# Performance work log

Hardware: AMD Instinct MI355X
Metric: run time of the kernel (lower is better)

The kernel has to match this reference:

```python
import jax, jax.numpy as jnp
import numpy as np

# dims (match init_kwargs)
B, S, HID = 2, 2048, 2048
NH = 16
DN = 128   # qk_nope_head_dim
DR = 64    # qk_rope_head_dim
DV = 128   # v_head_dim
QLR = 1536 # q_lora_rank
KVLR = 512 # kv_lora_rank
QHD = DN + DR  # 192
ROPE_BASE = 10000.0
EPS = 1e-6


def rms_norm(x, w):
    # ZeroCenteredRMSNorm: weight is zero-centered, scale = (1 + w)
    var = jnp.mean(x * x, axis=-1, keepdims=True)
    return x * jax.lax.rsqrt(var + EPS) * (1.0 + w)


def rotate_half(x):
    d = x.shape[-1] // 2
    return jnp.concatenate([-x[..., d:], x[..., :d]], axis=-1)


def deinterleave(x):
    # rearrange '(d_pairs two) -> (two d_pairs)'
    return jnp.concatenate([x[..., 0::2], x[..., 1::2]], axis=-1)


def setup_inputs() -> dict:
    key = jax.random.key(0)
    ks = jax.random.split(key, 8)
    s = 0.02
    return {
        "hidden_states": jax.random.normal(ks[0], (B, S, HID), jnp.float32),
        "position_ids": jnp.arange(S, dtype=jnp.int32),
        "Wq_down": jax.random.normal(ks[1], (HID, QLR), jnp.float32) * s,
        "q_norm_w": jnp.zeros((QLR,), jnp.float32),
        "Wq_up": jax.random.normal(ks[2], (QLR, NH * QHD), jnp.float32) * s,
        "Wkv_down": jax.random.normal(ks[3], (HID, KVLR + DR), jnp.float32) * s,
        "kv_norm_w": jnp.zeros((KVLR,), jnp.float32),
        "Wkv_up": jax.random.normal(ks[4], (KVLR, NH * (DN + DV)), jnp.float32) * s,
        "W_gate": jax.random.normal(ks[5], (HID, NH * DV), jnp.float32) * s,
        "W_out": jax.random.normal(ks[6], (NH * DV, HID), jnp.float32) * s,
    }


def reference(hidden_states, position_ids, Wq_down, q_norm_w, Wq_up,
              Wkv_down, kv_norm_w, Wkv_up, W_gate, W_out):
    bsz, q_len, _ = hidden_states.shape
    pos = jnp.broadcast_to(position_ids[None, :], (bsz, q_len))  # [b,s]

    # Q path: down-proj -> RMSNorm -> up-proj -> [b,h,s,QHD]
    q = rms_norm(hidden_states @ Wq_down, q_norm_w) @ Wq_up
    q = q.reshape(bsz, q_len, NH, QHD).transpose(0, 2, 1, 3)
    q_nope, q_rope = q[..., :DN], q[..., DN:]

    # KV path: joint down-proj -> split latent / rope key
    ckv = hidden_states @ Wkv_down                     # [b,s,KVLR+DR]
    c_kv, k_rope = ckv[..., :KVLR], ckv[..., KVLR:]
    k_rope = k_rope[:, None, :, :]                     # [b,1,s,DR]
    kv = rms_norm(c_kv, kv_norm_w) @ Wkv_up            # [b,s,NH*(DN+DV)]
    kv = kv.reshape(bsz, q_len, NH, DN + DV).transpose(0, 2, 1, 3)
    k_nope, v = kv[..., :DN], kv[..., DN:]

    # partial RoPE on rope dims (with the '(pairs two)->(two pairs)' permute)
    inv_freq = 1.0 / (ROPE_BASE ** (jnp.arange(0, DR, 2, dtype=jnp.float32) / DR))
    freqs = pos[..., None].astype(jnp.float32) * inv_freq  # [b,s,DR/2]
    emb = jnp.concatenate([freqs, freqs], axis=-1)          # [b,s,DR]
    cos = jnp.cos(emb)[:, None, :, :]                       # [b,1,s,DR]
    sin = jnp.sin(emb)[:, None, :, :]
    q_r = deinterleave(q_rope)
    k_r = deinterleave(k_rope)
    q_r = q_r * cos + rotate_half(q_r) * sin
    k_r = k_r * cos + rotate_half(k_r) * sin

    query = jnp.concatenate([q_nope, q_r], axis=-1)                       # [b,h,s,QHD]
    key = jnp.concatenate([k_nope, jnp.broadcast_to(k_r, k_nope.shape[:-1] + (DR,))], axis=-1)

    scores = jnp.einsum('bhqd,bhkd->bhqk', query, key) / np.sqrt(QHD)
    attn = jax.nn.softmax(scores, axis=-1)
    out = jnp.einsum('bhqk,bhkd->bhqd', attn, v)                          # [b,h,s,DV]
    out = out.transpose(0, 2, 1, 3)                                       # [b,s,h,DV]

    gate = jax.nn.sigmoid(hidden_states @ W_gate).reshape(bsz, q_len, NH, DV)
    out = (out * gate).reshape(bsz, q_len, NH * DV)
    return out @ W_out
```

## Files before the change

### kernel.cpp

```cpp
#include <hip/hip_runtime.h>
#include <math.h>

#define BT 2
#define SL 2048
#define HIDN 2048
#define NHEADS 16
#define DNOPE 128
#define DROPE 64
#define DVAL 128
#define QHEAD 192
#define QLRANK 1536
#define KVLRANK 512
#define TTOK (BT * SL)
#define FN 4224
#define FC_CKV 1536
#define FC_ROPE 2048
#define FC_GATE 2176

typedef unsigned short u16;
typedef u16 u16x4 __attribute__((ext_vector_type(4)));
typedef u16 u16x8 __attribute__((ext_vector_type(8)));
typedef short bf16x8 __attribute__((ext_vector_type(8)));
typedef float f32x4 __attribute__((ext_vector_type(4)));

__device__ __forceinline__ u16 f2b(float f) {
    union { float f; unsigned u; } v; v.f = f;
    unsigned r = v.u + 0x7FFFu + ((v.u >> 16) & 1u);
    return (u16)(r >> 16);
}
__device__ __forceinline__ float b2f(u16 h) {
    union { unsigned u; float f; } v; v.u = ((unsigned)h) << 16;
    return v.f;
}
__device__ __forceinline__ float fexp2(float x) {
    float r;
    asm("v_exp_f32 %0, %1" : "=v"(r) : "v"(x));
    return r;
}

__device__ __forceinline__ void gl2lds16(const u16* g, u16* l) {
    __builtin_amdgcn_global_load_lds((const __attribute__((address_space(1))) unsigned int*)g,
                                     (__attribute__((address_space(3))) unsigned int*)l, 16, 0, 0);
}

__device__ __forceinline__ void tcast_tile(const float* __restrict__ in, u16* __restrict__ out,
                                           int R, int C, int tx, int ty, int t) {
    __shared__ u16 tile[64][72];
    const int c0 = tx * 64, r0 = ty * 64;
    const int tr = t >> 4, tc4 = (t & 15) * 4;
#pragma unroll
    for (int i = 0; i < 4; ++i) {
        const int r = tr + i * 16;
        const float4 v = *(const float4*)&in[(size_t)(r0 + r) * C + c0 + tc4];
        u16x4 u;
        u.x = f2b(v.x); u.y = f2b(v.y); u.z = f2b(v.z); u.w = f2b(v.w);
        *(u16x4*)&tile[r][tc4] = u;
    }
    __syncthreads();
#pragma unroll
    for (int i = 0; i < 4; ++i) {
        const int rr = tr + i * 16;
        u16x4 u;
        u.x = tile[tc4 + 0][rr];
        u.y = tile[tc4 + 1][rr];
        u.z = tile[tc4 + 2][rr];
        u.w = tile[tc4 + 3][rr];
        *(u16x4*)&out[(size_t)(c0 + rr) * R + r0 + tc4] = u;
    }
}

__global__ __launch_bounds__(256) void precast_k(
    const float* __restrict__ Wq_down, const float* __restrict__ Wq_up,
    const float* __restrict__ Wkv_down, const float* __restrict__ Wkv_up,
    const float* __restrict__ W_gate, const float* __restrict__ W_out,
    const float* __restrict__ hs, u16* __restrict__ wqd_t, u16* __restrict__ wqu_t,
    u16* __restrict__ wkvd_t, u16* __restrict__ wkvu_t, u16* __restrict__ wg_t,
    u16* __restrict__ wo_t, u16* __restrict__ hs16) {
    const int tid = blockIdx.x;
    const int t = threadIdx.x;
    if (tid >= 4768) {
        int i = (tid - 4768) * 256 + t;
        for (; i < TTOK * HIDN / 4; i += 2048 * 256) {
            const float4 v = ((const float4*)hs)[i];
            u16x4 u;
            u.x = f2b(v.x); u.y = f2b(v.y); u.z = f2b(v.z); u.w = f2b(v.w);
            ((u16x4*)hs16)[i] = u;
        }
        return;
    }
    if (tid < 768) {
        tcast_tile(Wq_down, wqd_t, 2048, 1536, tid % 24, tid / 24, t);
    } else if (tid < 1920) {
        const int i = tid - 768;
        tcast_tile(Wq_up, wqu_t, 1536, 3072, i % 48, i / 48, t);
    } else if (tid < 2208) {
        const int i = tid - 1920;
        tcast_tile(Wkv_down, wkvd_t, 2048, 576, i % 9, i / 9, t);
    } else if (tid < 2720) {
        const int i = tid - 2208;
        tcast_tile(Wkv_up, wkvu_t, 512, 4096, i % 64, i / 64, t);
    } else if (tid < 3744) {
        const int i = tid - 2720;
        tcast_tile(W_gate, wg_t, 2048, 2048, i % 32, i / 32, t);
    } else {
        const int i = tid - 3744;
        tcast_tile(W_out, wo_t, 2048, 2048, i % 32, i / 32, t);
    }
}

template <int MODE>
__global__ __launch_bounds__(256) void gemm_bf16_k(const u16* __restrict__ A,
                                                   const u16* __restrict__ Bt,
                                                   void* __restrict__ Cv, u16* __restrict__ C2,
                                                   int M, int N, int K) {
    __shared__ u16 As[128 * 64];
    __shared__ u16 Bs[128 * 64];
    const int t = threadIdx.x;
    const int nx = gridDim.x;
    const int bid = blockIdx.x + nx * blockIdx.y;
    const int cpx = (nx * gridDim.y) >> 3;
    const int swz = (bid & 7) * cpx + (bid >> 3);
    const int bn = (swz % nx) * 128, bm = (swz / nx) * 128;
    const int w = t >> 6, lane = t & 63;
    const int wr = (w >> 1) * 64, wc = (w & 1) * 64;
    const int lr = lane & 15, lg = lane >> 4;

    const int srow = w * 32 + (lane >> 3);
    const int scol = ((lane & 7) ^ ((lane >> 3) & 7)) * 8;
    const u16* Ag = A + (size_t)(bm + srow) * K + scol;
    const u16* Bg = Bt + (size_t)(bn + srow) * K + scol;
    u16* Asl = As + w * 2048;
    u16* Bsl = Bs + w * 2048;

    f32x4 acc[4][4];
#pragma unroll
    for (int i = 0; i < 4; ++i)
#pragma unroll
        for (int j = 0; j < 4; ++j) acc[i][j] = 0.f;

    for (int k0 = 0; k0 < K; k0 += 64) {
        __syncthreads();
#pragma unroll
        for (int j = 0; j < 4; ++j) gl2lds16(Ag + (size_t)(j * 8) * K + k0, Asl + j * 512);
#pragma unroll
        for (int j = 0; j < 4; ++j) gl2lds16(Bg + (size_t)(j * 8) * K + k0, Bsl + j * 512);
        __syncthreads();
#pragma unroll
        for (int kk = 0; kk < 2; ++kk) {
            bf16x8 af[4], bfr[4];
#pragma unroll
            for (int mi = 0; mi < 4; ++mi) {
                const int row = wr + mi * 16 + lr;
                const int idx = (row * 64 + kk * 32 + lg * 8) ^ ((row & 7) << 3);
                af[mi] = *(const bf16x8*)&As[idx];
            }
#pragma unroll
            for (int ni = 0; ni < 4; ++ni) {
                const int row = wc + ni * 16 + lr;
                const int idx = (row * 64 + kk * 32 + lg * 8) ^ ((row & 7) << 3);
                bfr[ni] = *(const bf16x8*)&Bs[idx];
            }
#pragma unroll
            for (int mi = 0; mi < 4; ++mi)
#pragma unroll
                for (int ni = 0; ni < 4; ++ni)
                    acc[mi][ni] = __builtin_amdgcn_mfma_f32_16x16x32_bf16(af[mi], bfr[ni],
                                                                          acc[mi][ni], 0, 0, 0);
        }
    }
#pragma unroll
    for (int mi = 0; mi < 4; ++mi)
#pragma unroll
        for (int ni = 0; ni < 4; ++ni) {
            const int row0 = bm + wr + mi * 16 + lg * 4;
            const int col = bn + wc + ni * 16 + lr;
            if (MODE == 3) {
                const int h = col >> 8, cd = col & 255;
                if (cd < 128) {
#pragma unroll
                    for (int r = 0; r < 4; ++r)
                        ((u16*)Cv)[(size_t)(row0 + r) * 2048 + h * 128 + cd] =
                            f2b(acc[mi][ni][r]);
                } else {
                    u16x4 pk;
                    pk.x = f2b(acc[mi][ni][0]);
                    pk.y = f2b(acc[mi][ni][1]);
                    pk.z = f2b(acc[mi][ni][2]);
                    pk.w = f2b(acc[mi][ni][3]);
                    const int bb = row0 >> 11;
                    *(u16x4*)&C2[((size_t)((bb * 16 + h) * 128 + (cd - 128))) * SL +
                                 (row0 & (SL - 1))] = pk;
                }
            } else {
#pragma unroll
                for (int r = 0; r < 4; ++r) {
                    float v = acc[mi][ni][r];
                    if (MODE == 2 && col >= FC_GATE) v = 1.f / (1.f + __expf(-v));
                    if (MODE == 1)
                        ((float*)Cv)[(size_t)(row0 + r) * N + col] = v;
                    else
                        ((u16*)Cv)[(size_t)(row0 + r) * N + col] = f2b(v);
                }
            }
        }
}

__global__ __launch_bounds__(256) void rms2_k(const u16* __restrict__ fout,
                                              const float* __restrict__ qw,
                                              const float* __restrict__ kw, u16* __restrict__ qn,
                                              u16* __restrict__ kvn) {
    const int rid = blockIdx.x;
    const bool isq = rid < TTOK;
    const int row = isq ? rid : rid - TTOK;
    const int n = isq ? QLRANK : KVLRANK;
    const u16* x = fout + (size_t)row * FN + (isq ? 0 : FC_CKV);
    const float* w = isq ? qw : kw;
    u16* y = isq ? (qn + (size_t)row * QLRANK) : (kvn + (size_t)row * KVLRANK);
    const int t = threadIdx.x;
    float ss = 0.f;
    for (int d = t * 4; d < n; d += 1024) {
        const u16x4 u = *(const u16x4*)&x[d];
        const float a = b2f(u.x), b = b2f(u.y), c = b2f(u.z), e = b2f(u.w);
        ss += a * a + b * b + c * c + e * e;
    }
    ss += __shfl_down(ss, 32);
    ss += __shfl_down(ss, 16);
    ss += __shfl_down(ss, 8);
    ss += __shfl_down(ss, 4);
    ss += __shfl_down(ss, 2);
    ss += __shfl_down(ss, 1);
    __shared__ float red[5];
    if ((t & 63) == 0) red[t >> 6] = ss;
    __syncthreads();
    if (t == 0) red[4] = rsqrtf((red[0] + red[1] + red[2] + red[3]) / (float)n + 1e-6f);
    __syncthreads();
    const float sc = red[4];
    for (int d = t * 4; d < n; d += 1024) {
        const u16x4 u = *(const u16x4*)&x[d];
        const float4 wv = *(const float4*)&w[d];
        u16x4 o;
        o.x = f2b(b2f(u.x) * sc * (1.f + wv.x));
        o.y = f2b(b2f(u.y) * sc * (1.f + wv.y));
        o.z = f2b(b2f(u.z) * sc * (1.f + wv.z));
        o.w = f2b(b2f(u.w) * sc * (1.f + wv.w));
        *(u16x4*)&y[d] = o;
    }
}

__global__ __launch_bounds__(64) void rope_k(u16* __restrict__ q, const u16* __restrict__ fout,
                                             u16* __restrict__ kr, const int* __restrict__ pos_ids) {
    const int tok = blockIdx.x * 2 + (threadIdx.x >> 5);
    const int j = threadIdx.x & 31;
    const int s = tok & (SL - 1);
    const float pos = (float)pos_ids[s];
    const float inv = 1.f / powf(10000.f, (float)(2 * j) / 64.f);
    const float f = pos * inv;
    const float c = cosf(f), sn = sinf(f);
    const u16* kc = fout + (size_t)tok * FN + FC_ROPE;
    const unsigned kp = *(const unsigned*)&kc[2 * j];
    const float ke = b2f((u16)(kp & 0xffff)), ko = b2f((u16)(kp >> 16));
    kr[tok * 64 + j] = f2b(ke * c - ko * sn);
    kr[tok * 64 + 32 + j] = f2b(ko * c + ke * sn);
#pragma unroll
    for (int h = 0; h < NHEADS; ++h) {
        u16* qb = q + (size_t)tok * (NHEADS * QHEAD) + h * QHEAD + DNOPE;
        const unsigned qp = *(const unsigned*)&qb[2 * j];
        const float qe = b2f((u16)(qp & 0xffff)), qo = b2f((u16)(qp >> 16));
        qb[j] = f2b(qe * c - qo * sn);
        qb[32 + j] = f2b(qo * c + qe * sn);
    }
}

#define PSTR 76
__global__ __launch_bounds__(256, 2) void mla_attn_k(const u16* __restrict__ qbuf,
                                                     const u16* __restrict__ knope,
                                                     const u16* __restrict__ kr,
                                                     const u16* __restrict__ vT,
                                                     const u16* __restrict__ gateb,
                                                     u16* __restrict__ outg) {
    __shared__ u16 Ks[64 * 200];
    __shared__ u16 Vt[128 * 72];
    __shared__ u16 Ps[4 * 32 * PSTR];
    const int bh = blockIdx.x;
    const int b = bh >> 4, h = bh & 15;
    const int q0 = blockIdx.y * 128;
    const int t = threadIdx.x, w = t >> 6, lane = t & 63;
    const int lr = lane & 15, lg = lane >> 4;
    const float qs = 0.07216878364870322f * 1.4426950408889634f;
    const float THR = 8.f * 1.4426950408889634f;

    int kRow[6], kC8[6];
#pragma unroll
    for (int c = 0; c < 6; ++c) {
        const int i = t + c * 256;
        kRow[c] = i / 24;
        kC8[c] = (i % 24) * 8;
    }
    int vRow[4], vC8[4];
#pragma unroll
    for (int c = 0; c < 4; ++c) {
        const int i = t + c * 256;
        vRow[c] = i >> 3;
        vC8[c] = (i & 7) * 8;
    }

    bf16x8 aq[2][6];
#pragma unroll
    for (int mi = 0; mi < 2; ++mi) {
        const int qrow = b * SL + q0 + w * 32 + mi * 16 + lr;
#pragma unroll
        for (int ks = 0; ks < 6; ++ks) {
            const u16x8 raw = *(const u16x8*)&qbuf[(size_t)qrow * (NHEADS * QHEAD) + h * QHEAD +
                                                   ks * 32 + lg * 8];
            bf16x8 o;
#pragma unroll
            for (int j = 0; j < 8; ++j) o[j] = (short)f2b(b2f(raw[j]) * qs);
            aq[mi][ks] = o;
        }
    }

    f32x4 O[2][8];
#pragma unroll
    for (int mi = 0; mi < 2; ++mi)
#pragma unroll
        for (int df = 0; df < 8; ++df) O[mi][df] = 0.f;
    float m[2][4], l[2][4];
#pragma unroll
    for (int mi = 0; mi < 2; ++mi)
#pragma unroll
        for (int r = 0; r < 4; ++r) {
            m[mi][r] = -INFINITY;
            l[mi][r] = 0.f;
        }

    u16x8 kreg[6], vreg[4];
#define ATTN_ISSUE_K(K0)                                                                     \
    {                                                                                        \
        _Pragma("unroll") for (int c = 0; c < 6; ++c) {                                      \
            const int tok = b * SL + (K0) + kRow[c];                                         \
            kreg[c] = (kC8[c] < 128)                                                         \
                          ? *(const u16x8*)&knope[(size_t)tok * 2048 + h * 128 + kC8[c]]     \
                          : *(const u16x8*)&kr[(size_t)tok * 64 + (kC8[c] - 128)];           \
        }                                                                                    \
    }
#define ATTN_ISSUE_V(K0)                                                                     \
    {                                                                                        \
        _Pragma("unroll") for (int c = 0; c < 4; ++c)                                        \
            vreg[c] = *(const u16x8*)&vT[(size_t)(bh * 128 + vRow[c]) * SL + (K0) + vC8[c]]; \
    }

    ATTN_ISSUE_K(0);
    ATTN_ISSUE_V(0);

    for (int it = 0; it < SL / 64; ++it) {
        __syncthreads();
#pragma unroll
        for (int c = 0; c < 6; ++c) *(u16x8*)&Ks[kRow[c] * 200 + kC8[c]] = kreg[c];
#pragma unroll
        for (int c = 0; c < 4; ++c) *(u16x8*)&Vt[vRow[c] * 72 + vC8[c]] = vreg[c];
        __syncthreads();
        const bool more = (it + 1) < SL / 64;
        const int kn = (it + 1) * 64;
        if (more) ATTN_ISSUE_K(kn);

        f32x4 s[2][4];
#pragma unroll
        for (int mi = 0; mi < 2; ++mi)
#pragma unroll
            for (int nf = 0; nf < 4; ++nf) s[mi][nf] = 0.f;
#pragma unroll
        for (int ks = 0; ks < 6; ++ks) {
#pragma unroll
            for (int nf = 0; nf < 4; ++nf) {
                const bf16x8 bk = *(const bf16x8*)&Ks[(nf * 16 + lr) * 200 + ks * 32 + lg * 8];
                s[0][nf] = __builtin_amdgcn_mfma_f32_16x16x32_bf16(aq[0][ks], bk, s[0][nf], 0, 0, 0);
                s[1][nf] = __builtin_amdgcn_mfma_f32_16x16x32_bf16(aq[1][ks], bk, s[1][nf], 0, 0, 0);
            }
        }

        float lmv[2][4];
        float growth = -INFINITY;
#pragma unroll
        for (int mi = 0; mi < 2; ++mi)
#pragma unroll
            for (int r = 0; r < 4; ++r) {
                float lm = fmaxf(fmaxf(s[mi][0][r], s[mi][1][r]), fmaxf(s[mi][2][r], s[mi][3][r]));
                lm = fmaxf(lm, __shfl_xor(lm, 1));
                lm = fmaxf(lm, __shfl_xor(lm, 2));
                lm = fmaxf(lm, __shfl_xor(lm, 4));
                lm = fmaxf(lm, __shfl_xor(lm, 8));
                lmv[mi][r] = lm;
                growth = fmaxf(growth, lm - m[mi][r]);
            }
        const bool skip = __all(growth <= THR);

#pragma unroll
        for (int mi = 0; mi < 2; ++mi) {
            const int pb = w * 32 * PSTR + mi * 16 * PSTR;
#pragma unroll
            for (int r = 0; r < 4; ++r) {
                const float mn = skip ? m[mi][r] : fmaxf(m[mi][r], lmv[mi][r]);
                float p0 = fexp2(s[mi][0][r] - mn);
                float p1 = fexp2(s[mi][1][r] - mn);
                float p2 = fexp2(s[mi][2][r] - mn);
                float p3 = fexp2(s[mi][3][r] - mn);
                float ps = (p0 + p1) + (p2 + p3);
                ps += __shfl_xor(ps, 1);
                ps += __shfl_xor(ps, 2);
                ps += __shfl_xor(ps, 4);
                ps += __shfl_xor(ps, 8);
                if (skip) {
                    l[mi][r] += ps;
                } else {
                    const float al = fexp2(m[mi][r] - mn);
                    l[mi][r] = l[mi][r] * al + ps;
                    m[mi][r] = mn;
#pragma unroll
                    for (int df = 0; df < 8; ++df) O[mi][df][r] *= al;
                }
                const int prow = pb + (lg * 4 + r) * PSTR + lr;
                Ps[prow] = f2b(p0);
                Ps[prow + 16] = f2b(p1);
                Ps[prow + 32] = f2b(p2);
                Ps[prow + 48] = f2b(p3);
            }
        }

        if (more) ATTN_ISSUE_V(kn);

        bf16x8 pa[2][2];
#pragma unroll
        for (int mi = 0; mi < 2; ++mi)
#pragma unroll
            for (int ks2 = 0; ks2 < 2; ++ks2)
                pa[mi][ks2] =
                    *(const bf16x8*)&Ps[w * 32 * PSTR + (mi * 16 + lr) * PSTR + ks2 * 32 + lg * 8];
#pragma unroll
        for (int df = 0; df < 8; ++df)
#pragma unroll
            for (int ks2 = 0; ks2 < 2; ++ks2) {
                const bf16x8 bv = *(const bf16x8*)&Vt[(df * 16 + lr) * 72 + ks2 * 32 + lg * 8];
                O[0][df] = __builtin_amdgcn_mfma_f32_16x16x32_bf16(pa[0][ks2], bv, O[0][df], 0, 0, 0);
                O[1][df] = __builtin_amdgcn_mfma_f32_16x16x32_bf16(pa[1][ks2], bv, O[1][df], 0, 0, 0);
            }
    }
#pragma unroll
    for (int mi = 0; mi < 2; ++mi) {
        float invl[4];
#pragma unroll
        for (int r = 0; r < 4; ++r) invl[r] = 1.f / l[mi][r];
#pragma unroll
        for (int df = 0; df < 8; ++df)
#pragma unroll
            for (int r = 0; r < 4; ++r) {
                const int qq = b * SL + q0 + w * 32 + mi * 16 + lg * 4 + r;
                const int col = h * DVAL + df * 16 + lr;
                const float o = O[mi][df][r] * invl[r];
                const float g = b2f(gateb[(size_t)qq * FN + col]);
                outg[(size_t)qq * (NHEADS * DVAL) + col] = f2b(o * g);
            }
    }
}

extern "C" void kernel_launch(void* const* d_in, const int* in_sizes, int n_in, void* d_out,
                              int out_size, void* d_ws, size_t ws_size, hipStream_t stream) {
    const float* hs = (const float*)d_in[0];
    const int* pos = (const int*)d_in[1];
    const float* Wq_down = (const float*)d_in[2];
    const float* q_norm_w = (const float*)d_in[3];
    const float* Wq_up = (const float*)d_in[4];
    const float* Wkv_down = (const float*)d_in[5];
    const float* kv_norm_w = (const float*)d_in[6];
    const float* Wkv_up = (const float*)d_in[7];
    const float* W_gate = (const float*)d_in[8];
    const float* W_out = (const float*)d_in[9];
    float* out = (float*)d_out;

    u16* p = (u16*)d_ws;
    u16* hs16 = p;      p += (size_t)TTOK * HIDN;
    u16* wdown_t = p;   p += (size_t)FN * HIDN;
    u16* wqd_t = wdown_t;
    u16* wkvd_t = wdown_t + (size_t)QLRANK * HIDN;
    u16* wg_t = wdown_t + (size_t)FC_GATE * HIDN;
    u16* wqu_t = p;     p += (size_t)(NHEADS * QHEAD) * QLRANK;
    u16* wkvu_t = p;    p += (size_t)(NHEADS * 256) * KVLRANK;
    u16* wo_t = p;      p += (size_t)HIDN * (NHEADS * DVAL);
    u16* fout = p;      p += (size_t)TTOK * FN;
    u16* qdownN = p;    p += (size_t)TTOK * QLRANK;
    u16* qbuf = p;      p += (size_t)TTOK * (NHEADS * QHEAD);
    u16* kvn = p;       p += (size_t)TTOK * KVLRANK;
    u16* knope = p;     p += (size_t)TTOK * (NHEADS * DNOPE);
    u16* krb = p;       p += (size_t)TTOK * DROPE;
    u16* vTg = p;       p += (size_t)32 * 128 * SL;
    u16* outg = p;      p += (size_t)TTOK * (NHEADS * DVAL);

    const dim3 blk(256);

    precast_k<<<dim3(6816), blk, 0, stream>>>(Wq_down, Wq_up, Wkv_down, Wkv_up, W_gate, W_out, hs,
                                              wqd_t, wqu_t, wkvd_t, wkvu_t, wg_t, wo_t, hs16);

    gemm_bf16_k<2><<<dim3(FN / 128, TTOK / 128), blk, 0, stream>>>(hs16, wdown_t, fout, nullptr,
                                                                   TTOK, FN, HIDN);
    rms2_k<<<dim3(2 * TTOK), blk, 0, stream>>>(fout, q_norm_w, kv_norm_w, qdownN, kvn);
    gemm_bf16_k<0><<<dim3((NHEADS * QHEAD) / 128, TTOK / 128), blk, 0, stream>>>(
        qdownN, wqu_t, qbuf, nullptr, TTOK, NHEADS * QHEAD, QLRANK);
    gemm_bf16_k<3><<<dim3((NHEADS * 256) / 128, TTOK / 128), blk, 0, stream>>>(
        kvn, wkvu_t, knope, vTg, TTOK, NHEADS * 256, KVLRANK);
    rope_k<<<dim3(TTOK / 2), dim3(64), 0, stream>>>(qbuf, fout, krb, pos);

    mla_attn_k<<<dim3(32, SL / 128), blk, 0, stream>>>(qbuf, knope, krb, vTg, fout + FC_GATE, outg);

    gemm_bf16_k<1><<<dim3(HIDN / 128, TTOK / 128), blk, 0, stream>>>(outg, wo_t, out, nullptr, TTOK,
                                                                     HIDN, NHEADS * DVAL);
}
```

Measured before the change: 466.0 us.

## Use 256x128 tiles with double-buffered LDS prefetch in bf16 GEMMs

Replaces the 128x128, 256-thread GEMM with a 256x128, 512-thread kernel. LDS is double-buffered so the next K tile's global-to-LDS loads are in flight while MFMAs run on the current tile, with explicit vmcnt waits and barriers. This targets exposed load latency and the two barriers per K step that the old single-buffer loop paid. In exchange, LDS use per block grows to 96KB and the grid gets fewer blocks (e.g. 16x16 for the output projection), which may hurt occupancy and wave balance across CUs.

```diff
diff --git a/kernel.cpp b/kernel.cpp
--- a/kernel.cpp
+++ b/kernel.cpp
@@ -109,71 +109,91 @@
 }
 
 template <int MODE>
-__global__ __launch_bounds__(256) void gemm_bf16_k(const u16* __restrict__ A,
-                                                   const u16* __restrict__ Bt,
-                                                   void* __restrict__ Cv, u16* __restrict__ C2,
-                                                   int M, int N, int K) {
-    __shared__ u16 As[128 * 64];
-    __shared__ u16 Bs[128 * 64];
+__global__ __launch_bounds__(512) void gemm256_k(const u16* __restrict__ A,
+                                                 const u16* __restrict__ Bt,
+                                                 void* __restrict__ Cv, u16* __restrict__ C2,
+                                                 int M, int N, int K) {
+    __shared__ u16 As[2][256 * 64];
+    __shared__ u16 Bs[2][128 * 64];
     const int t = threadIdx.x;
     const int nx = gridDim.x;
     const int bid = blockIdx.x + nx * blockIdx.y;
     const int cpx = (nx * gridDim.y) >> 3;
     const int swz = (bid & 7) * cpx + (bid >> 3);
-    const int bn = (swz % nx) * 128, bm = (swz / nx) * 128;
+    const int bn = (swz % nx) * 128, bm = (swz / nx) * 256;
     const int w = t >> 6, lane = t & 63;
-    const int wr = (w >> 1) * 64, wc = (w & 1) * 64;
+    const int wrow = (w >> 2) * 128, wcol = (w & 3) * 32;
     const int lr = lane & 15, lg = lane >> 4;
 
-    const int srow = w * 32 + (lane >> 3);
-    const int scol = ((lane & 7) ^ ((lane >> 3) & 7)) * 8;
-    const u16* Ag = A + (size_t)(bm + srow) * K + scol;
-    const u16* Bg = Bt + (size_t)(bn + srow) * K + scol;
-    u16* Asl = As + w * 2048;
-    u16* Bsl = Bs + w * 2048;
-
-    f32x4 acc[4][4];
-#pragma unroll
-    for (int i = 0; i < 4; ++i)
-#pragma unroll
-        for (int j = 0; j < 4; ++j) acc[i][j] = 0.f;
-
-    for (int k0 = 0; k0 < K; k0 += 64) {
-        __syncthreads();
-#pragma unroll
-        for (int j = 0; j < 4; ++j) gl2lds16(Ag + (size_t)(j * 8) * K + k0, Asl + j * 512);
-#pragma unroll
-        for (int j = 0; j < 4; ++j) gl2lds16(Bg + (size_t)(j * 8) * K + k0, Bsl + j * 512);
-        __syncthreads();
+    const int lrow = lane >> 3;
+    const int scol = ((lane & 7) ^ (lrow & 7)) * 8;
+    const u16* Ag = A + (size_t)(bm + w * 32 + lrow) * K + scol;
+    const u16* Bg = Bt + (size_t)(bn + w * 16 + lrow) * K + scol;
+
+#define STAGE256(kt, bsel)                                                           \
+    {                                                                                \
+        u16* ad = &As[bsel][w * 2048];                                               \
+        u16* bd = &Bs[bsel][w * 1024];                                               \
+        _Pragma("unroll") for (int j = 0; j < 4; ++j)                                \
+            gl2lds16(Ag + (size_t)(j * 8) * K + (size_t)(kt) * 64, ad + j * 512);    \
+        _Pragma("unroll") for (int j = 0; j < 2; ++j)                                \
+            gl2lds16(Bg + (size_t)(j * 8) * K + (size_t)(kt) * 64, bd + j * 512);    \
+    }
+
+    f32x4 acc[8][2];
+#pragma unroll
+    for (int i = 0; i < 8; ++i)
+#pragma unroll
+        for (int j = 0; j < 2; ++j) acc[i][j] = 0.f;
+
+    const int nt = K >> 6;
+    STAGE256(0, 0);
+    for (int kt = 0; kt < nt; ++kt) {
+        const int cur = kt & 1;
+        if (kt + 1 < nt) {
+            STAGE256(kt + 1, cur ^ 1);
+            asm volatile("s_waitcnt vmcnt(6)" ::: "memory");
+        } else {
+            asm volatile("s_waitcnt vmcnt(0)" ::: "memory");
+        }
+        __builtin_amdgcn_sched_barrier(0);
+        __builtin_amdgcn_s_barrier();
+        __builtin_amdgcn_sched_barrier(0);
 #pragma unroll
         for (int kk = 0; kk < 2; ++kk) {
-            bf16x8 af[4], bfr[4];
-#pragma unroll
-            for (int mi = 0; mi < 4; ++mi) {
-                const int row = wr + mi * 16 + lr;
+            bf16x8 af[8], bfr[2];
+#pragma unroll
+            for (int mi = 0; mi < 8; ++mi) {
+                const int row = wrow + mi * 16 + lr;
                 const int idx = (row * 64 + kk * 32 + lg * 8) ^ ((row & 7) << 3);
-                af[mi] = *(const bf16x8*)&As[idx];
-            }
-#pragma unroll
-            for (int ni = 0; ni < 4; ++ni) {
-                const int row = wc + ni * 16 + lr;
+                af[mi] = *(const bf16x8*)&As[cur][idx];
+            }
+#pragma unroll
+            for (int ni = 0; ni < 2; ++ni) {
+                const int row = wcol + ni * 16 + lr;
                 const int idx = (row * 64 + kk * 32 + lg * 8) ^ ((row & 7) << 3);
-                bfr[ni] = *(const bf16x8*)&Bs[idx];
-            }
-#pragma unroll
-            for (int mi = 0; mi < 4; ++mi)
-#pragma unroll
-                for (int ni = 0; ni < 4; ++ni)
+                bfr[ni] = *(const bf16x8*)&Bs[cur][idx];
+            }
+#pragma unroll
+            for (int mi = 0; mi < 8; ++mi)
+#pragma unroll
+                for (int ni = 0; ni < 2; ++ni)
                     acc[mi][ni] = __builtin_amdgcn_mfma_f32_16x16x32_bf16(af[mi], bfr[ni],
                                                                           acc[mi][ni], 0, 0, 0);
         }
-    }
-#pragma unroll
-    for (int mi = 0; mi < 4; ++mi)
-#pragma unroll
-        for (int ni = 0; ni < 4; ++ni) {
-            const int row0 = bm + wr + mi * 16 + lg * 4;
-            const int col = bn + wc + ni * 16 + lr;
+        asm volatile("s_waitcnt lgkmcnt(0)" ::: "memory");
+        __builtin_amdgcn_sched_barrier(0);
+        __builtin_amdgcn_s_barrier();
+        __builtin_amdgcn_sched_barrier(0);
+    }
+#undef STAGE256
+
+#pragma unroll
+    for (int mi = 0; mi < 8; ++mi)
+#pragma unroll
+        for (int ni = 0; ni < 2; ++ni) {
+            const int row0 = bm + wrow + mi * 16 + lg * 4;
+            const int col = bn + wcol + ni * 16 + lr;
             if (MODE == 3) {
                 const int h = col >> 8, cd = col & 255;
                 if (cd < 128) {
@@ -495,21 +515,22 @@
     u16* outg = p;      p += (size_t)TTOK * (NHEADS * DVAL);
 
     const dim3 blk(256);
+    const dim3 blk512(512);
 
     precast_k<<<dim3(6816), blk, 0, stream>>>(Wq_down, Wq_up, Wkv_down, Wkv_up, W_gate, W_out, hs,
                                               wqd_t, wqu_t, wkvd_t, wkvu_t, wg_t, wo_t, hs16);
 
-    gemm_bf16_k<2><<<dim3(FN / 128, TTOK / 128), blk, 0, stream>>>(hs16, wdown_t, fout, nullptr,
-                                                                   TTOK, FN, HIDN);
+    gemm256_k<2><<<dim3(FN / 128, TTOK / 256), blk512, 0, stream>>>(hs16, wdown_t, fout, nullptr,
+                                                                    TTOK, FN, HIDN);
     rms2_k<<<dim3(2 * TTOK), blk, 0, stream>>>(fout, q_norm_w, kv_norm_w, qdownN, kvn);
-    gemm_bf16_k<0><<<dim3((NHEADS * QHEAD) / 128, TTOK / 128), blk, 0, stream>>>(
+    gemm256_k<0><<<dim3((NHEADS * QHEAD) / 128, TTOK / 256), blk512, 0, stream>>>(
         qdownN, wqu_t, qbuf, nullptr, TTOK, NHEADS * QHEAD, QLRANK);
-    gemm_bf16_k<3><<<dim3((NHEADS * 256) / 128, TTOK / 128), blk, 0, stream>>>(
+    gemm256_k<3><<<dim3((NHEADS * 256) / 128, TTOK / 256), blk512, 0, stream>>>(
         kvn, wkvu_t, knope, vTg, TTOK, NHEADS * 256, KVLRANK);
     rope_k<<<dim3(TTOK / 2), dim3(64), 0, stream>>>(qbuf, fout, krb, pos);
 
     mla_attn_k<<<dim3(32, SL / 128), blk, 0, stream>>>(qbuf, knope, krb, vTg, fout + FC_GATE, outg);
 
-    gemm_bf16_k<1><<<dim3(HIDN / 128, TTOK / 128), blk, 0, stream>>>(outg, wo_t, out, nullptr, TTOK,
-                                                                     HIDN, NHEADS * DVAL);
-}
+    gemm256_k<1><<<dim3(HIDN / 128, TTOK / 256), blk512, 0, stream>>>(outg, wo_t, out, nullptr,
+                                                                      TTOK, HIDN, NHEADS * DVAL);
+}
```

Result: slower. 489.2 us (+5.0%).
